# Optimization experiments

Hardware: AMD Instinct MI355X
Metric: run time of the kernel (lower is better)

Reference implementation:

```python
import jax, jax.numpy as jnp
import numpy as np

EPS = 1e-5
NEG_SLOPE = 0.01  # nn.LeakyReLU default


def _bn(x, gamma, beta, mean, var):
    # eval-mode batchnorm over last (channel) axis
    return (x - mean) * (gamma * jax.lax.rsqrt(var + EPS)) + beta


def setup_inputs() -> dict:
    key = jax.random.key(0)
    ks = jax.random.split(key, 12)
    B, N, F = 4, 256, 128
    Cin = 2 * F + 2  # edge channels (2) + pairwise concat (2F)
    inp = {
        "node_feat": jax.random.normal(ks[0], (B, N, F), jnp.float32),
        "edge_feat": jax.random.normal(ks[1], (B, N, N, 2), jnp.float32),
        # conv1: 1x1, (2F+2) -> F, no bias
        "w1": jax.random.normal(ks[2], (F, Cin), jnp.float32) * (1.0 / np.sqrt(Cin)),
        "bn1_gamma": jnp.ones((F,), jnp.float32),
        "bn1_beta": jnp.zeros((F,), jnp.float32),
        "bn1_mean": jnp.zeros((F,), jnp.float32),
        "bn1_var": jnp.ones((F,), jnp.float32),
        # conv2: 1x1, F -> F, no bias
        "w2": jax.random.normal(ks[3], (F, F), jnp.float32) * (1.0 / np.sqrt(F)),
        "bn2_gamma": jnp.ones((F,), jnp.float32),
        "bn2_beta": jnp.zeros((F,), jnp.float32),
        "bn2_mean": jnp.zeros((F,), jnp.float32),
        "bn2_var": jnp.ones((F,), jnp.float32),
        # pair_network: Linear(F, 2)
        "pw": jax.random.normal(ks[4], (2, F), jnp.float32) * (1.0 / np.sqrt(F)),
        "pb": jax.random.uniform(ks[5], (2,), jnp.float32, -0.1, 0.1),
    }
    return inp


def reference(node_feat, edge_feat, w1, bn1_gamma, bn1_beta, bn1_mean, bn1_var,
              w2, bn2_gamma, bn2_beta, bn2_mean, bn2_var, pw, pb):
    # node_feat: [B,N,F], edge_feat: [B,N,N,2]
    F = node_feat.shape[-1]
    # concat order along channels: [edge (2), P_left (F), P_right (F)]
    w_e = w1[:, :2]            # [F, 2]
    w_l = w1[:, 2:2 + F]       # [F, F]
    w_r = w1[:, 2 + F:]        # [F, F]
    # Fused broadcast-GEMM: conv1x1 over concat == sum of partial projections.
    hl = jnp.einsum('bif,gf->big', node_feat, w_l)   # [B,N,F] (row/left term)
    hr = jnp.einsum('bjf,gf->bjg', node_feat, w_r)   # [B,N,F] (col/right term)
    he = jnp.einsum('bijc,gc->bijg', edge_feat, w_e)  # [B,N,N,F]
    h = he + hl[:, :, None, :] + hr[:, None, :, :]    # [B,N,N,F]
    h = _bn(h, bn1_gamma, bn1_beta, bn1_mean, bn1_var)
    h = jnp.where(h >= 0, h, NEG_SLOPE * h)           # LeakyReLU
    # Dropout is identity in eval mode.
    h = jnp.einsum('bijf,gf->bijg', h, w2)            # conv2 1x1
    h = _bn(h, bn2_gamma, bn2_beta, bn2_mean, bn2_var)
    out = jnp.einsum('bijf,of->bijo', h, pw) + pb     # [B,N,N,2]
    return out
```

## Files before the change

kernel.cpp:

```cpp
#include <hip/hip_runtime.h>

#define EPS    1e-5f
#define NSLOPE 0.01f
#define B 4
#define N 256
#define F 128

#define WS_WE0 0
#define WS_WE1 128
#define WS_PF0 256
#define WS_PF1 384
#define WS_C   512
#define WS_HL  1024
#define WS_HR  (WS_HL + B*N*F)

__global__ __launch_bounds__(128) void prep_all(
    const float* __restrict__ node, const float* __restrict__ w1,
    const float* __restrict__ g1, const float* __restrict__ b1,
    const float* __restrict__ m1, const float* __restrict__ v1,
    const float* __restrict__ w2, const float* __restrict__ g2,
    const float* __restrict__ b2, const float* __restrict__ m2,
    const float* __restrict__ v2, const float* __restrict__ pw,
    const float* __restrict__ pb, float* __restrict__ ws) {
  if (blockIdx.x == 256) {
    __shared__ float s2s[F], t2s[F];
    int g = threadIdx.x;
    float s1v = g1[g] / sqrtf(v1[g] + EPS);
    ws[WS_WE0 + g] = w1[g * 258 + 0] * s1v;
    ws[WS_WE1 + g] = w1[g * 258 + 1] * s1v;
    float s2v = g2[g] / sqrtf(v2[g] + EPS);
    s2s[g] = s2v;
    t2s[g] = b2[g] - m2[g] * s2v;
    __syncthreads();
    float a0 = 0.f, a1 = 0.f;
    for (int f = 0; f < F; ++f) {
      float wv = w2[f * F + g];
      a0 = fmaf(pw[f]     * s2s[f], wv, a0);
      a1 = fmaf(pw[F + f] * s2s[f], wv, a1);
    }
    ws[WS_PF0 + g] = a0;
    ws[WS_PF1 + g] = a1;
    if (g < 2) {
      float c = pb[g];
      for (int f = 0; f < F; ++f) c += pw[g * F + f] * t2s[f];
      ws[WS_C + g] = c;
    }
    return;
  }
  __shared__ float4 ns4[64 * 32];
  int t = threadIdx.x;
  int rc = blockIdx.x >> 4;
  int gc = blockIdx.x & 15;
  int r0 = rc * 64;
  const float4* node4 = reinterpret_cast<const float4*>(node) + (size_t)r0 * 32;
  #pragma unroll
  for (int k = 0; k < 16; ++k) {
    int L = k * 128 + t;
    int row = L >> 5, s = L & 31;
    ns4[row * 32 + (s ^ (row & 7))] = node4[L];
  }
  __syncthreads();
  int lane = t & 63;
  int wv = __builtin_amdgcn_readfirstlane(t >> 6);
  int g0 = gc * 8 + wv * 4;
  int lbase = lane * 32;
  int lx = lane & 7;
  float accl[4] = {0.f, 0.f, 0.f, 0.f};
  float accr[4] = {0.f, 0.f, 0.f, 0.f};
  #pragma unroll 8
  for (int q = 0; q < 32; ++q) {
    float4 nv = ns4[lbase + (q ^ lx)];
    #pragma unroll
    for (int k = 0; k < 4; ++k) {
      const float* wrow = w1 + (size_t)(g0 + k) * 258;
      float2 wl0 = *reinterpret_cast<const float2*>(wrow + 2 + 4 * q);
      float2 wl1 = *reinterpret_cast<const float2*>(wrow + 4 + 4 * q);
      float2 wr0 = *reinterpret_cast<const float2*>(wrow + 130 + 4 * q);
      float2 wr1 = *reinterpret_cast<const float2*>(wrow + 132 + 4 * q);
      accl[k] = fmaf(nv.x, wl0.x, accl[k]);
      accl[k] = fmaf(nv.y, wl0.y, accl[k]);
      accl[k] = fmaf(nv.z, wl1.x, accl[k]);
      accl[k] = fmaf(nv.w, wl1.y, accl[k]);
      accr[k] = fmaf(nv.x, wr0.x, accr[k]);
      accr[k] = fmaf(nv.y, wr0.y, accr[k]);
      accr[k] = fmaf(nv.z, wr1.x, accr[k]);
      accr[k] = fmaf(nv.w, wr1.y, accr[k]);
    }
  }
  int row = r0 + lane;
  float4 ol, orr;
  #pragma unroll
  for (int k = 0; k < 4; ++k) {
    int g = g0 + k;
    float s1v = g1[g] / sqrtf(v1[g] + EPS);
    float t1v = b1[g] - m1[g] * s1v;
    (&ol.x)[k]  = fmaf(accl[k], s1v, t1v);
    (&orr.x)[k] = accr[k] * s1v;
  }
  *reinterpret_cast<float4*>(ws + WS_HL + (size_t)row * F + g0) = ol;
  *reinterpret_cast<float4*>(ws + WS_HR + (size_t)row * F + g0) = orr;
}

__global__ __launch_bounds__(256) void fused_main(
    const float* __restrict__ edge,
    const float* __restrict__ ws, float* __restrict__ out) {
  __shared__ float hls[32][132];
  __shared__ float hrs[32][132];
  int b = blockIdx.z, i0 = blockIdx.y * 32, j0 = blockIdx.x * 32;
  int t = threadIdx.x;
  int ti = t >> 4, tj = t & 15;
  int i1 = i0 + ti, i2 = i1 + 16, j1 = j0 + tj, j2 = j1 + 16;
  float2 e00 = *reinterpret_cast<const float2*>(edge + ((size_t)(b * N + i1) * N + j1) * 2);
  float2 e01 = *reinterpret_cast<const float2*>(edge + ((size_t)(b * N + i1) * N + j2) * 2);
  float2 e10 = *reinterpret_cast<const float2*>(edge + ((size_t)(b * N + i2) * N + j1) * 2);
  float2 e11 = *reinterpret_cast<const float2*>(edge + ((size_t)(b * N + i2) * N + j2) * 2);
  {
    const float* hl = ws + WS_HL;
    const float* hr = ws + WS_HR;
    int r = t >> 3, cq = (t & 7) * 16;
    const float* sl = hl + (size_t)(b * N + i0 + r) * F + cq;
    const float* sr = hr + (size_t)(b * N + j0 + r) * F + cq;
    #pragma unroll
    for (int k = 0; k < 4; ++k) {
      *reinterpret_cast<float4*>(&hls[r][cq + 4 * k]) =
          *reinterpret_cast<const float4*>(sl + 4 * k);
      *reinterpret_cast<float4*>(&hrs[r][cq + 4 * k]) =
          *reinterpret_cast<const float4*>(sr + 4 * k);
    }
  }
  __syncthreads();
  const float4* W0p = reinterpret_cast<const float4*>(ws + WS_WE0);
  const float4* W1p = reinterpret_cast<const float4*>(ws + WS_WE1);
  const float4* P0p = reinterpret_cast<const float4*>(ws + WS_PF0);
  const float4* P1p = reinterpret_cast<const float4*>(ws + WS_PF1);
  float a00x = 0.f, a00y = 0.f, a01x = 0.f, a01y = 0.f;
  float a10x = 0.f, a10y = 0.f, a11x = 0.f, a11y = 0.f;
  #pragma unroll 4
  for (int gq = 0; gq < F / 4; ++gq) {
    int g = gq * 4;
    float4 L0 = *reinterpret_cast<const float4*>(&hls[ti][g]);
    float4 L1 = *reinterpret_cast<const float4*>(&hls[ti + 16][g]);
    float4 R0 = *reinterpret_cast<const float4*>(&hrs[tj][g]);
    float4 R1 = *reinterpret_cast<const float4*>(&hrs[tj + 16][g]);
    float4 W0 = W0p[gq];
    float4 W1 = W1p[gq];
    float4 P0 = P0p[gq];
    float4 P1 = P1p[gq];
#define DO_COMP(K)                                                             \
    {                                                                          \
      float w0 = W0.K, w1v = W1.K, p0 = P0.K, p1 = P1.K;                       \
      float v;                                                                 \
      v = L0.K + R0.K; v = fmaf(e00.x, w0, v); v = fmaf(e00.y, w1v, v);        \
      v = fmaxf(v, NSLOPE * v);                                                \
      a00x = fmaf(p0, v, a00x); a00y = fmaf(p1, v, a00y);                      \
      v = L0.K + R1.K; v = fmaf(e01.x, w0, v); v = fmaf(e01.y, w1v, v);        \
      v = fmaxf(v, NSLOPE * v);                                                \
      a01x = fmaf(p0, v, a01x); a01y = fmaf(p1, v, a01y);                      \
      v = L1.K + R0.K; v = fmaf(e10.x, w0, v); v = fmaf(e10.y, w1v, v);        \
      v = fmaxf(v, NSLOPE * v);                                                \
      a10x = fmaf(p0, v, a10x); a10y = fmaf(p1, v, a10y);                      \
      v = L1.K + R1.K; v = fmaf(e11.x, w0, v); v = fmaf(e11.y, w1v, v);        \
      v = fmaxf(v, NSLOPE * v);                                                \
      a11x = fmaf(p0, v, a11x); a11y = fmaf(p1, v, a11y);                      \
    }
    DO_COMP(x) DO_COMP(y) DO_COMP(z) DO_COMP(w)
#undef DO_COMP
  }
  float c0 = ws[WS_C + 0], c1 = ws[WS_C + 1];
  float2 o;
  o.x = a00x + c0; o.y = a00y + c1;
  *reinterpret_cast<float2*>(out + ((size_t)(b * N + i1) * N + j1) * 2) = o;
  o.x = a01x + c0; o.y = a01y + c1;
  *reinterpret_cast<float2*>(out + ((size_t)(b * N + i1) * N + j2) * 2) = o;
  o.x = a10x + c0; o.y = a10y + c1;
  *reinterpret_cast<float2*>(out + ((size_t)(b * N + i2) * N + j1) * 2) = o;
  o.x = a11x + c0; o.y = a11y + c1;
  *reinterpret_cast<float2*>(out + ((size_t)(b * N + i2) * N + j2) * 2) = o;
}

extern "C" void kernel_launch(void* const* d_in, const int* in_sizes, int n_in,
                              void* d_out, int out_size, void* d_ws, size_t ws_size,
                              hipStream_t stream) {
  const float* node = (const float*)d_in[0];
  const float* edge = (const float*)d_in[1];
  const float* w1   = (const float*)d_in[2];
  const float* g1   = (const float*)d_in[3];
  const float* b1   = (const float*)d_in[4];
  const float* m1   = (const float*)d_in[5];
  const float* v1   = (const float*)d_in[6];
  const float* w2   = (const float*)d_in[7];
  const float* g2   = (const float*)d_in[8];
  const float* b2   = (const float*)d_in[9];
  const float* m2   = (const float*)d_in[10];
  const float* v2   = (const float*)d_in[11];
  const float* pw   = (const float*)d_in[12];
  const float* pb   = (const float*)d_in[13];
  float* ws  = (float*)d_ws;
  float* out = (float*)d_out;

  prep_all<<<257, 128, 0, stream>>>(node, w1, g1, b1, m1, v1, w2, g2, b2, m2,
                                    v2, pw, pb, ws);
  fused_main<<<dim3(N / 32, N / 32, B), 256, 0, stream>>>(edge, ws, out);
}
```

Before: 30.96 us.

## Stage w1 slices in LDS for prep and use 512-thread main blocks

After: 25.61 us (median of 2 runs). 1.21x faster.

```diff
diff --git a/kernel.cpp b/kernel.cpp
--- a/kernel.cpp
+++ b/kernel.cpp
@@ -48,10 +48,12 @@
     return;
   }
   __shared__ float4 ns4[64 * 32];
+  __shared__ float  wlds[2][8][F];
   int t = threadIdx.x;
   int rc = blockIdx.x >> 4;
   int gc = blockIdx.x & 15;
   int r0 = rc * 64;
+  int gb = gc * 8;
   const float4* node4 = reinterpret_cast<const float4*>(node) + (size_t)r0 * 32;
   #pragma unroll
   for (int k = 0; k < 16; ++k) {
@@ -59,35 +61,39 @@
     int row = L >> 5, s = L & 31;
     ns4[row * 32 + (s ^ (row & 7))] = node4[L];
   }
+  #pragma unroll
+  for (int k = 0; k < 8; ++k) {
+    const float* wrow = w1 + (size_t)(gb + k) * 258;
+    wlds[0][k][t] = wrow[2 + t];
+    wlds[1][k][t] = wrow[130 + t];
+  }
   __syncthreads();
   int lane = t & 63;
   int wv = __builtin_amdgcn_readfirstlane(t >> 6);
-  int g0 = gc * 8 + wv * 4;
+  int lx = lane & 7;
   int lbase = lane * 32;
-  int lx = lane & 7;
   float accl[4] = {0.f, 0.f, 0.f, 0.f};
   float accr[4] = {0.f, 0.f, 0.f, 0.f};
-  #pragma unroll 8
+  #pragma unroll 4
   for (int q = 0; q < 32; ++q) {
     float4 nv = ns4[lbase + (q ^ lx)];
     #pragma unroll
     for (int k = 0; k < 4; ++k) {
-      const float* wrow = w1 + (size_t)(g0 + k) * 258;
-      float2 wl0 = *reinterpret_cast<const float2*>(wrow + 2 + 4 * q);
-      float2 wl1 = *reinterpret_cast<const float2*>(wrow + 4 + 4 * q);
-      float2 wr0 = *reinterpret_cast<const float2*>(wrow + 130 + 4 * q);
-      float2 wr1 = *reinterpret_cast<const float2*>(wrow + 132 + 4 * q);
-      accl[k] = fmaf(nv.x, wl0.x, accl[k]);
-      accl[k] = fmaf(nv.y, wl0.y, accl[k]);
-      accl[k] = fmaf(nv.z, wl1.x, accl[k]);
-      accl[k] = fmaf(nv.w, wl1.y, accl[k]);
-      accr[k] = fmaf(nv.x, wr0.x, accr[k]);
-      accr[k] = fmaf(nv.y, wr0.y, accr[k]);
-      accr[k] = fmaf(nv.z, wr1.x, accr[k]);
-      accr[k] = fmaf(nv.w, wr1.y, accr[k]);
+      int kk = wv * 4 + k;
+      float4 wl = *reinterpret_cast<const float4*>(&wlds[0][kk][q * 4]);
+      float4 wr = *reinterpret_cast<const float4*>(&wlds[1][kk][q * 4]);
+      accl[k] = fmaf(nv.x, wl.x, accl[k]);
+      accl[k] = fmaf(nv.y, wl.y, accl[k]);
+      accl[k] = fmaf(nv.z, wl.z, accl[k]);
+      accl[k] = fmaf(nv.w, wl.w, accl[k]);
+      accr[k] = fmaf(nv.x, wr.x, accr[k]);
+      accr[k] = fmaf(nv.y, wr.y, accr[k]);
+      accr[k] = fmaf(nv.z, wr.z, accr[k]);
+      accr[k] = fmaf(nv.w, wr.w, accr[k]);
     }
   }
   int row = r0 + lane;
+  int g0 = gb + wv * 4;
   float4 ol, orr;
   #pragma unroll
   for (int k = 0; k < 4; ++k) {
@@ -101,7 +107,7 @@
   *reinterpret_cast<float4*>(ws + WS_HR + (size_t)row * F + g0) = orr;
 }
 
-__global__ __launch_bounds__(256) void fused_main(
+__global__ __launch_bounds__(512) void fused_main(
     const float* __restrict__ edge,
     const float* __restrict__ ws, float* __restrict__ out) {
   __shared__ float hls[32][132];
@@ -109,37 +115,28 @@
   int b = blockIdx.z, i0 = blockIdx.y * 32, j0 = blockIdx.x * 32;
   int t = threadIdx.x;
   int ti = t >> 4, tj = t & 15;
-  int i1 = i0 + ti, i2 = i1 + 16, j1 = j0 + tj, j2 = j1 + 16;
-  float2 e00 = *reinterpret_cast<const float2*>(edge + ((size_t)(b * N + i1) * N + j1) * 2);
-  float2 e01 = *reinterpret_cast<const float2*>(edge + ((size_t)(b * N + i1) * N + j2) * 2);
-  float2 e10 = *reinterpret_cast<const float2*>(edge + ((size_t)(b * N + i2) * N + j1) * 2);
-  float2 e11 = *reinterpret_cast<const float2*>(edge + ((size_t)(b * N + i2) * N + j2) * 2);
+  int i1 = i0 + ti, j1 = j0 + tj, j2 = j1 + 16;
+  float2 e0 = *reinterpret_cast<const float2*>(edge + ((size_t)(b * N + i1) * N + j1) * 2);
+  float2 e1 = *reinterpret_cast<const float2*>(edge + ((size_t)(b * N + i1) * N + j2) * 2);
   {
-    const float* hl = ws + WS_HL;
-    const float* hr = ws + WS_HR;
-    int r = t >> 3, cq = (t & 7) * 16;
-    const float* sl = hl + (size_t)(b * N + i0 + r) * F + cq;
-    const float* sr = hr + (size_t)(b * N + j0 + r) * F + cq;
-    #pragma unroll
-    for (int k = 0; k < 4; ++k) {
-      *reinterpret_cast<float4*>(&hls[r][cq + 4 * k]) =
-          *reinterpret_cast<const float4*>(sl + 4 * k);
-      *reinterpret_cast<float4*>(&hrs[r][cq + 4 * k]) =
-          *reinterpret_cast<const float4*>(sr + 4 * k);
-    }
+    int r = t >> 4, c0 = (t & 15) * 8;
+    const float* sl = ws + WS_HL + (size_t)(b * N + i0 + r) * F + c0;
+    const float* sr = ws + WS_HR + (size_t)(b * N + j0 + r) * F + c0;
+    *reinterpret_cast<float4*>(&hls[r][c0])     = *reinterpret_cast<const float4*>(sl);
+    *reinterpret_cast<float4*>(&hls[r][c0 + 4]) = *reinterpret_cast<const float4*>(sl + 4);
+    *reinterpret_cast<float4*>(&hrs[r][c0])     = *reinterpret_cast<const float4*>(sr);
+    *reinterpret_cast<float4*>(&hrs[r][c0 + 4]) = *reinterpret_cast<const float4*>(sr + 4);
   }
   __syncthreads();
   const float4* W0p = reinterpret_cast<const float4*>(ws + WS_WE0);
   const float4* W1p = reinterpret_cast<const float4*>(ws + WS_WE1);
   const float4* P0p = reinterpret_cast<const float4*>(ws + WS_PF0);
   const float4* P1p = reinterpret_cast<const float4*>(ws + WS_PF1);
-  float a00x = 0.f, a00y = 0.f, a01x = 0.f, a01y = 0.f;
-  float a10x = 0.f, a10y = 0.f, a11x = 0.f, a11y = 0.f;
+  float a0x = 0.f, a0y = 0.f, a1x = 0.f, a1y = 0.f;
   #pragma unroll 4
   for (int gq = 0; gq < F / 4; ++gq) {
     int g = gq * 4;
-    float4 L0 = *reinterpret_cast<const float4*>(&hls[ti][g]);
-    float4 L1 = *reinterpret_cast<const float4*>(&hls[ti + 16][g]);
+    float4 L  = *reinterpret_cast<const float4*>(&hls[ti][g]);
     float4 R0 = *reinterpret_cast<const float4*>(&hrs[tj][g]);
     float4 R1 = *reinterpret_cast<const float4*>(&hrs[tj + 16][g]);
     float4 W0 = W0p[gq];
@@ -150,32 +147,22 @@
     {                                                                          \
       float w0 = W0.K, w1v = W1.K, p0 = P0.K, p1 = P1.K;                       \
       float v;                                                                 \
-      v = L0.K + R0.K; v = fmaf(e00.x, w0, v); v = fmaf(e00.y, w1v, v);        \
+      v = L.K + R0.K; v = fmaf(e0.x, w0, v); v = fmaf(e0.y, w1v, v);           \
       v = fmaxf(v, NSLOPE * v);                                                \
-      a00x = fmaf(p0, v, a00x); a00y = fmaf(p1, v, a00y);                      \
-      v = L0.K + R1.K; v = fmaf(e01.x, w0, v); v = fmaf(e01.y, w1v, v);        \
+      a0x = fmaf(p0, v, a0x); a0y = fmaf(p1, v, a0y);                          \
+      v = L.K + R1.K; v = fmaf(e1.x, w0, v); v = fmaf(e1.y, w1v, v);           \
       v = fmaxf(v, NSLOPE * v);                                                \
-      a01x = fmaf(p0, v, a01x); a01y = fmaf(p1, v, a01y);                      \
-      v = L1.K + R0.K; v = fmaf(e10.x, w0, v); v = fmaf(e10.y, w1v, v);        \
-      v = fmaxf(v, NSLOPE * v);                                                \
-      a10x = fmaf(p0, v, a10x); a10y = fmaf(p1, v, a10y);                      \
-      v = L1.K + R1.K; v = fmaf(e11.x, w0, v); v = fmaf(e11.y, w1v, v);        \
-      v = fmaxf(v, NSLOPE * v);                                                \
-      a11x = fmaf(p0, v, a11x); a11y = fmaf(p1, v, a11y);                      \
+      a1x = fmaf(p0, v, a1x); a1y = fmaf(p1, v, a1y);                          \
     }
     DO_COMP(x) DO_COMP(y) DO_COMP(z) DO_COMP(w)
 #undef DO_COMP
   }
   float c0 = ws[WS_C + 0], c1 = ws[WS_C + 1];
   float2 o;
-  o.x = a00x + c0; o.y = a00y + c1;
+  o.x = a0x + c0; o.y = a0y + c1;
   *reinterpret_cast<float2*>(out + ((size_t)(b * N + i1) * N + j1) * 2) = o;
-  o.x = a01x + c0; o.y = a01y + c1;
+  o.x = a1x + c0; o.y = a1y + c1;
   *reinterpret_cast<float2*>(out + ((size_t)(b * N + i1) * N + j2) * 2) = o;
-  o.x = a10x + c0; o.y = a10y + c1;
-  *reinterpret_cast<float2*>(out + ((size_t)(b * N + i2) * N + j1) * 2) = o;
-  o.x = a11x + c0; o.y = a11y + c1;
-  *reinterpret_cast<float2*>(out + ((size_t)(b * N + i2) * N + j2) * 2) = o;
 }
 
 extern "C" void kernel_launch(void* const* d_in, const int* in_sizes, int n_in,
@@ -200,5 +187,5 @@
 
   prep_all<<<257, 128, 0, stream>>>(node, w1, g1, b1, m1, v1, w2, g2, b2, m2,
                                     v2, pw, pb, ws);
-  fused_main<<<dim3(N / 32, N / 32, B), 256, 0, stream>>>(edge, ws, out);
+  fused_main<<<dim3(N / 32, N / 32, B), 512, 0, stream>>>(edge, ws, out);
 }
```
